# Kernel optimization log

Measured on AMD Instinct MI355X. Metric: run time of the kernel, lower is better.

## Reference

```python
import jax, jax.numpy as jnp
import numpy as np

B, S, E = 4, 2048, 1024
H = 16
DH = E // H  # per-head qk and v projection dim (64)


def setup_inputs() -> dict:
    key = jax.random.key(0)
    ks = jax.random.split(key, 12)
    sc = lambda fan_in: 1.0 / np.sqrt(fan_in)
    inp = {
        "query": jax.random.normal(ks[0], (B, S, E), jnp.float32),
        "key": jax.random.normal(ks[1], (B, S, E), jnp.float32),
        "value": jax.random.normal(ks[2], (B, S, E), jnp.float32),
        "attention_bias": jax.random.normal(ks[3], (S, S), jnp.float32),
        # stacked per-head Linear weights/biases (H independent heads in original)
        "Wq": jax.random.uniform(ks[4], (H, E, DH), jnp.float32, -sc(E), sc(E)),
        "bq": jax.random.uniform(ks[5], (H, DH), jnp.float32, -sc(E), sc(E)),
        "Wk": jax.random.uniform(ks[6], (H, E, DH), jnp.float32, -sc(E), sc(E)),
        "bk": jax.random.uniform(ks[7], (H, DH), jnp.float32, -sc(E), sc(E)),
        "Wv": jax.random.uniform(ks[8], (H, E, DH), jnp.float32, -sc(E), sc(E)),
        "bv": jax.random.uniform(ks[9], (H, DH), jnp.float32, -sc(E), sc(E)),
        "Wo": jax.random.uniform(ks[10], (H * DH, E), jnp.float32, -sc(H * DH), sc(H * DH)),
        "bo": jax.random.uniform(ks[11], (E,), jnp.float32, -sc(H * DH), sc(H * DH)),
    }
    return inp


def reference(query, key, value, attention_bias, Wq, bq, Wk, bk, Wv, bv, Wo, bo):
    # Batched equivalent of per-head Linear projections + per-head SDPA.
    q = jnp.einsum("bse,hed->bhsd", query, Wq) + bq[None, :, None, :]   # (B,H,S,DH)
    k = jnp.einsum("bte,hed->bhtd", key, Wk) + bk[None, :, None, :]     # (B,H,S,DH)
    v = jnp.einsum("bte,hed->bhtd", value, Wv) + bv[None, :, None, :]   # (B,H,S,DH)
    scale = 1.0 / jnp.sqrt(jnp.asarray(DH, q.dtype))
    scores = jnp.einsum("bhsd,bhtd->bhst", q, k) * scale                # (B,H,S,S)
    scores = scores + attention_bias[None, None, :, :]
    attn = jax.nn.softmax(scores, axis=-1)
    # dropout_p = 0.0 -> no dropout
    ctx = jnp.einsum("bhst,bhtd->bhsd", attn, v)                        # (B,H,S,DH)
    concat = ctx.transpose(0, 2, 1, 3).reshape(B, S, H * DH)            # (B,S,H*DH)
    return concat @ Wo + bo                                             # (B,S,E)
```

## Files before the change

### kernel.cpp

```cpp
#include <hip/hip_runtime.h>

#define S_LEN 2048
#define E_DIM 1024
#define H_NUM 16

typedef __attribute__((ext_vector_type(8))) short s16x8;
typedef __attribute__((ext_vector_type(4))) float f32x4;
typedef __attribute__((ext_vector_type(4))) _Float16 h16x4;

#define GA(p) ((__attribute__((address_space(1))) void*)(p))
#define LA(p) ((__attribute__((address_space(3))) void*)(p))

#define LOG2E 1.4426950408889634f
#define SCALE_Q (0.125f * LOG2E)
#define SHIFT 12.0f

union cvt16 { int4 v; s16x8 s8; short e[8]; };

__device__ __forceinline__ short f2bf(float f) {
  union { float f; unsigned u; } v; v.f = f;
  unsigned r = v.u + 0x7FFFu + ((v.u >> 16) & 1u);
  return (short)(r >> 16);
}
__device__ __forceinline__ short f2bf_fast(float f) {
  union { float f; unsigned u; } v; v.f = f;
  return (short)((v.u + 0x8000u) >> 16);
}

__global__ void transpose_cast(const float* __restrict__ src, short* __restrict__ dst,
                               int R, int C, long sbs, long dbs, float scale) {
  __shared__ float tile[32][33];
  const float* s = src + (long)blockIdx.z * sbs;
  short* d = dst + (long)blockIdx.z * dbs;
  int c0 = blockIdx.x * 32, r0 = blockIdx.y * 32;
  #pragma unroll
  for (int i = threadIdx.y; i < 32; i += 8)
    tile[i][threadIdx.x] = s[(long)(r0 + i) * C + c0 + threadIdx.x];
  __syncthreads();
  #pragma unroll
  for (int i = threadIdx.y; i < 32; i += 8)
    d[(long)(c0 + i) * R + r0 + threadIdx.x] = f2bf(tile[threadIdx.x][i] * scale);
}

__global__ void bias_rearrange(const float* __restrict__ bias, _Float16* __restrict__ biasR) {
  long tg = (long)blockIdx.x * 256 + threadIdx.x;
  long o = tg * 4;
  int q = (int)(o >> 11);
  int t = (int)(o & 2047);
  int b64 = t & ~63, u = t & 63, ln = u >> 2;
  const float* src = bias + (long)q * 2048 + b64 + ln;
  h16x4 hv;
  #pragma unroll
  for (int nt = 0; nt < 4; ++nt) hv[nt] = (_Float16)src[nt * 16];
  *(h16x4*)(biasR + o) = hv;
}

__global__ __launch_bounds__(256, 3) void proj_gemm(
    const float* __restrict__ Aq, const float* __restrict__ Ak, const float* __restrict__ Av,
    const short* __restrict__ Bt,
    const float* __restrict__ bq, const float* __restrict__ bk, const float* __restrict__ bv,
    short* __restrict__ qkOut, short* __restrict__ VT) {
  __shared__ float Asub[128 * 64];
  __shared__ short Bsub[128 * 64];
  const int tid = threadIdx.x;
  const int w = tid >> 6, lane = tid & 63, ln = lane & 15, quad = lane >> 4;
  const int row0 = blockIdx.x * 128, n0 = blockIdx.y * 128;
  const int seg = n0 >> 10;
  const float* A = (seg == 0) ? Aq : ((seg == 1) ? Ak : Av);
  const float* bptr = (seg == 0) ? bq : ((seg == 1) ? bk : bv);
  const float bscale = (seg == 0) ? SCALE_Q : 1.0f;
  const int nloc = n0 & 1023;
  const int wm = (w & 1) * 64, wn = (w >> 1) * 64;

  f32x4 acc[4][4];
  #pragma unroll
  for (int i = 0; i < 4; ++i)
    #pragma unroll
    for (int j = 0; j < 4; ++j) acc[i][j] = (f32x4){0.f, 0.f, 0.f, 0.f};

  for (int kt = 0; kt < 16; ++kt) {
    const int k0 = kt * 64;
    #pragma unroll
    for (int j = 0; j < 4; ++j) {
      int ci = (w * 4 + j) * 64 + lane;
      int r = ci >> 3, s = ci & 7, g = s ^ (r & 7);
      const short* gb = Bt + (long)(n0 + r) * 1024 + k0 + g * 8;
      __builtin_amdgcn_global_load_lds(GA(gb), LA(&Bsub[ci * 8]), 16, 0, 0);
    }
    #pragma unroll
    for (int it = 0; it < 8; ++it) {
      int ci = it * 256 + tid;
      int r = ci >> 4, s = ci & 15, g = (s & 8) | ((s & 7) ^ (r & 7));
      const float* ga = A + (long)(row0 + r) * 1024 + k0 + g * 4;
      __builtin_amdgcn_global_load_lds(GA(ga), LA(&Asub[ci * 4]), 16, 0, 0);
    }
    __syncthreads();
    #pragma unroll
    for (int kk = 0; kk < 2; ++kk) {
      s16x8 af[4], bfr[4];
      #pragma unroll
      for (int i = 0; i < 4; ++i) {
        int ra = wm + i * 16 + ln;
        int c0 = kk * 8 + quad * 2;
        int s0 = (c0 & 8) | ((c0 & 7) ^ (ra & 7));
        int c1 = c0 + 1;
        int s1 = (c1 & 8) | ((c1 & 7) ^ (ra & 7));
        f32x4 lo = *(const f32x4*)&Asub[ra * 64 + s0 * 4];
        f32x4 hi = *(const f32x4*)&Asub[ra * 64 + s1 * 4];
        s16x8 t;
        t[0] = f2bf(lo[0]); t[1] = f2bf(lo[1]); t[2] = f2bf(lo[2]); t[3] = f2bf(lo[3]);
        t[4] = f2bf(hi[0]); t[5] = f2bf(hi[1]); t[6] = f2bf(hi[2]); t[7] = f2bf(hi[3]);
        af[i] = t;
      }
      #pragma unroll
      for (int j = 0; j < 4; ++j) {
        int rb = wn + j * 16 + ln;
        int slot = (kk * 4 + quad) ^ (rb & 7);
        bfr[j] = *(const s16x8*)&Bsub[rb * 64 + slot * 8];
      }
      #pragma unroll
      for (int i = 0; i < 4; ++i)
        #pragma unroll
        for (int j = 0; j < 4; ++j)
          acc[i][j] = __builtin_amdgcn_mfma_f32_16x16x32_bf16(af[i], bfr[j], acc[i][j], 0, 0, 0);
    }
    __syncthreads();
  }
  if (seg < 2) {
    #pragma unroll
    for (int j = 0; j < 4; ++j) {
      float bvj = bptr[nloc + wn + j * 16 + ln] * bscale;
      int n = n0 + wn + j * 16 + ln;
      #pragma unroll
      for (int i = 0; i < 4; ++i)
        #pragma unroll
        for (int r = 0; r < 4; ++r) {
          int row = row0 + wm + i * 16 + quad * 4 + r;
          qkOut[(long)row * 2048 + n] = f2bf(acc[i][j][r] + bvj);
        }
    }
  } else {
    #pragma unroll
    for (int j = 0; j < 4; ++j) {
      int nl = nloc + wn + j * 16 + ln;
      int hh = nl >> 6, d = nl & 63;
      float bvj = bptr[nl];
      #pragma unroll
      for (int i = 0; i < 4; ++i) {
        int row = row0 + wm + i * 16 + quad * 4;
        int b = row >> 11, t = row & 2047;
        short4 sv;
        sv.x = f2bf(acc[i][j][0] + bvj);
        sv.y = f2bf(acc[i][j][1] + bvj);
        sv.z = f2bf(acc[i][j][2] + bvj);
        sv.w = f2bf(acc[i][j][3] + bvj);
        *(short4*)&VT[((long)(b * 16 + hh) * 64 + d) * 2048 + t] = sv;
      }
    }
  }
}

__global__ __launch_bounds__(256, 3) void flash_attn(
    const short* __restrict__ qk, const short* __restrict__ VT,
    const _Float16* __restrict__ biasR, short* __restrict__ concat) {
  __shared__ short Ks[2][4096];
  __shared__ short Vs[2][4096];
  __shared__ short Ps[128 * 72];
  const int tid = threadIdx.x;
  const int w = tid >> 6, lane = tid & 63, ln = lane & 15, quad = lane >> 4;
  const int q0 = blockIdx.x * 128;
  const int h = blockIdx.y, bb = blockIdx.z;

  s16x8 ones;
  #pragma unroll
  for (int e = 0; e < 8; ++e) ones[e] = (short)0x3F80;

  s16x8 qf[2][2];
  const short* qbase = qk + (long)(bb * 2048 + q0 + w * 32) * 2048 + h * 64;
  #pragma unroll
  for (int i = 0; i < 2; ++i)
    #pragma unroll
    for (int kk = 0; kk < 2; ++kk) {
      cvt16 u; u.v = *(const int4*)(qbase + (long)(i * 16 + ln) * 2048 + kk * 32 + quad * 8);
      qf[i][kk] = u.s8;
    }

  f32x4 o[2][4], lacc[2];
  #pragma unroll
  for (int i = 0; i < 2; ++i) {
    #pragma unroll
    for (int nt = 0; nt < 4; ++nt) o[i][nt] = (f32x4){0.f, 0.f, 0.f, 0.f};
    lacc[i] = (f32x4){0.f, 0.f, 0.f, 0.f};
  }

  const short* kbase = qk + (long)bb * 2048 * 2048 + 1024 + h * 64;
  const short* vbase = VT + (long)(bb * 16 + h) * 64 * 2048;
  const _Float16* bbase = biasR + (long)(q0 + w * 32 + quad * 4) * 2048 + ln * 4;

  #pragma unroll
  for (int j = 0; j < 2; ++j) {
    int ci = (w * 2 + j) * 64 + lane;
    int r = ci >> 3, cs = (ci & 7) ^ (r & 7);
    __builtin_amdgcn_global_load_lds(GA(kbase + (long)r * 2048 + cs * 8), LA(&Ks[0][(w * 2 + j) * 512]), 16, 0, 0);
    __builtin_amdgcn_global_load_lds(GA(vbase + (long)r * 2048 + cs * 8), LA(&Vs[0][(w * 2 + j) * 512]), 16, 0, 0);
  }

  for (int kv = 0; kv < 32; ++kv) {
    const int t0 = kv * 64, b = kv & 1;
    __syncthreads();

    h16x4 bld[2][4];
    #pragma unroll
    for (int i = 0; i < 2; ++i)
      #pragma unroll
      for (int r = 0; r < 4; ++r)
        bld[i][r] = *(const h16x4*)(bbase + (long)(i * 16 + r) * 2048 + t0);
    __builtin_amdgcn_sched_barrier(0);

    if (kv < 31) {
      const short* kb = kbase + (long)(t0 + 64) * 2048;
      const short* vb = vbase + (t0 + 64);
      #pragma unroll
      for (int j = 0; j < 2; ++j) {
        int ci = (w * 2 + j) * 64 + lane;
        int r = ci >> 3, cs = (ci & 7) ^ (r & 7);
        __builtin_amdgcn_global_load_lds(GA(kb + (long)r * 2048 + cs * 8), LA(&Ks[b ^ 1][(w * 2 + j) * 512]), 16, 0, 0);
        __builtin_amdgcn_global_load_lds(GA(vb + (long)r * 2048 + cs * 8), LA(&Vs[b ^ 1][(w * 2 + j) * 512]), 16, 0, 0);
      }
    }

    f32x4 sa[2][4];
    #pragma unroll
    for (int i = 0; i < 2; ++i)
      #pragma unroll
      for (int nt = 0; nt < 4; ++nt) sa[i][nt] = (f32x4){-SHIFT, -SHIFT, -SHIFT, -SHIFT};
    #pragma unroll
    for (int kk = 0; kk < 2; ++kk) {
      s16x8 bfr[4];
      #pragma unroll
      for (int nt = 0; nt < 4; ++nt)
        bfr[nt] = *(const s16x8*)&Ks[b][((nt * 16 + ln) << 6) + (((kk * 4 + quad) ^ (ln & 7)) << 3)];
      #pragma unroll
      for (int i = 0; i < 2; ++i)
        #pragma unroll
        for (int nt = 0; nt < 4; ++nt)
          sa[i][nt] = __builtin_amdgcn_mfma_f32_16x16x32_bf16(qf[i][kk], bfr[nt], sa[i][nt], 0, 0, 0);
    }

    #pragma unroll
    for (int i = 0; i < 2; ++i)
      #pragma unroll
      for (int r = 0; r < 4; ++r) {
        #pragma unroll
        for (int nt = 0; nt < 4; ++nt) {
          float bb_ = (float)bld[i][r][nt];
          float p = __builtin_amdgcn_exp2f(fmaf(bb_, LOG2E, sa[i][nt][r]));
          Ps[(w * 32 + i * 16 + quad * 4 + r) * 72 + nt * 16 + ln] = f2bf_fast(p);
        }
      }

    #pragma unroll
    for (int kk = 0; kk < 2; ++kk) {
      s16x8 pa[2], vbf[4];
      #pragma unroll
      for (int i = 0; i < 2; ++i)
        pa[i] = *(const s16x8*)&Ps[(w * 32 + i * 16 + ln) * 72 + kk * 32 + quad * 8];
      #pragma unroll
      for (int nt = 0; nt < 4; ++nt)
        vbf[nt] = *(const s16x8*)&Vs[b][((nt * 16 + ln) << 6) + (((kk * 4 + quad) ^ (ln & 7)) << 3)];
      #pragma unroll
      for (int i = 0; i < 2; ++i) {
        #pragma unroll
        for (int nt = 0; nt < 4; ++nt)
          o[i][nt] = __builtin_amdgcn_mfma_f32_16x16x32_bf16(pa[i], vbf[nt], o[i][nt], 0, 0, 0);
        lacc[i] = __builtin_amdgcn_mfma_f32_16x16x32_bf16(pa[i], ones, lacc[i], 0, 0, 0);
      }
    }
  }

  #pragma unroll
  for (int i = 0; i < 2; ++i) {
    float inv[4];
    #pragma unroll
    for (int r = 0; r < 4; ++r) inv[r] = __builtin_amdgcn_rcpf(lacc[i][r]);
    long rowb = (long)bb * 2048 + q0 + w * 32 + i * 16 + quad * 4;
    #pragma unroll
    for (int nt = 0; nt < 4; ++nt)
      #pragma unroll
      for (int r = 0; r < 4; ++r)
        concat[(rowb + r) * 1024 + h * 64 + nt * 16 + ln] = f2bf(o[i][nt][r] * inv[r]);
  }
}

__global__ __launch_bounds__(256, 3) void out_gemm(
    const short* __restrict__ A, const short* __restrict__ Bt,
    const float* __restrict__ bo, float* __restrict__ Cout) {
  __shared__ short Asub[128 * 64];
  __shared__ short Bsub[128 * 64];
  const int tid = threadIdx.x;
  const int w = tid >> 6, lane = tid & 63, ln = lane & 15, quad = lane >> 4;
  const int row0 = blockIdx.x * 128, n0 = blockIdx.y * 128;
  const int wm = (w & 1) * 64, wn = (w >> 1) * 64;

  f32x4 acc[4][4];
  #pragma unroll
  for (int i = 0; i < 4; ++i)
    #pragma unroll
    for (int j = 0; j < 4; ++j) acc[i][j] = (f32x4){0.f, 0.f, 0.f, 0.f};

  for (int kt = 0; kt < 16; ++kt) {
    const int k0 = kt * 64;
    #pragma unroll
    for (int j = 0; j < 4; ++j) {
      int ci = (w * 4 + j) * 64 + lane;
      int r = ci >> 3, s = ci & 7, g = s ^ (r & 7);
      const short* ga = A + (long)(row0 + r) * 1024 + k0 + g * 8;
      __builtin_amdgcn_global_load_lds(GA(ga), LA(&Asub[ci * 8]), 16, 0, 0);
      const short* gb = Bt + (long)(n0 + r) * 1024 + k0 + g * 8;
      __builtin_amdgcn_global_load_lds(GA(gb), LA(&Bsub[ci * 8]), 16, 0, 0);
    }
    __syncthreads();
    #pragma unroll
    for (int kk = 0; kk < 2; ++kk) {
      s16x8 af[4], bfr[4];
      #pragma unroll
      for (int i = 0; i < 4; ++i) {
        int ra = wm + i * 16 + ln;
        int slot = (kk * 4 + quad) ^ (ra & 7);
        af[i] = *(const s16x8*)&Asub[ra * 64 + slot * 8];
      }
      #pragma unroll
      for (int j = 0; j < 4; ++j) {
        int rb = wn + j * 16 + ln;
        int slot = (kk * 4 + quad) ^ (rb & 7);
        bfr[j] = *(const s16x8*)&Bsub[rb * 64 + slot * 8];
      }
      #pragma unroll
      for (int i = 0; i < 4; ++i)
        #pragma unroll
        for (int j = 0; j < 4; ++j)
          acc[i][j] = __builtin_amdgcn_mfma_f32_16x16x32_bf16(af[i], bfr[j], acc[i][j], 0, 0, 0);
    }
    __syncthreads();
  }
  #pragma unroll
  for (int j = 0; j < 4; ++j) {
    int n = n0 + wn + j * 16 + ln;
    float bvj = bo[n];
    #pragma unroll
    for (int i = 0; i < 4; ++i)
      #pragma unroll
      for (int r = 0; r < 4; ++r) {
        int row = row0 + wm + i * 16 + quad * 4 + r;
        Cout[(long)row * 1024 + n] = acc[i][j][r] + bvj;
      }
  }
}

extern "C" void kernel_launch(void* const* d_in, const int* in_sizes, int n_in,
                              void* d_out, int out_size, void* d_ws, size_t ws_size,
                              hipStream_t stream) {
  const float* query = (const float*)d_in[0];
  const float* key_  = (const float*)d_in[1];
  const float* value = (const float*)d_in[2];
  const float* abias = (const float*)d_in[3];
  const float* Wq = (const float*)d_in[4];
  const float* bq = (const float*)d_in[5];
  const float* Wk = (const float*)d_in[6];
  const float* bk = (const float*)d_in[7];
  const float* Wv = (const float*)d_in[8];
  const float* bv = (const float*)d_in[9];
  const float* Wo = (const float*)d_in[10];
  const float* bo = (const float*)d_in[11];
  float* out = (float*)d_out;

  char* ws = (char*)d_ws;
  short*    WqkvT  = (short*)(ws);
  _Float16* biasR  = (_Float16*)(ws);
  short*    qk     = (short*)(ws + 8388608);
  short*    VT     = (short*)(ws + 41943040);
  short*    WoT    = (short*)(ws + 41943040);
  short*    concat = (short*)(ws + 58720256);

  dim3 tb(32, 8);
  transpose_cast<<<dim3(2, 32, 16), tb, 0, stream>>>(Wq, WqkvT,           1024, 64, 65536L, 65536L, SCALE_Q);
  transpose_cast<<<dim3(2, 32, 16), tb, 0, stream>>>(Wk, WqkvT + 1048576, 1024, 64, 65536L, 65536L, 1.0f);
  transpose_cast<<<dim3(2, 32, 16), tb, 0, stream>>>(Wv, WqkvT + 2097152, 1024, 64, 65536L, 65536L, 1.0f);
  proj_gemm<<<dim3(64, 24), 256, 0, stream>>>(query, key_, value, WqkvT, bq, bk, bv, qk, VT);
  bias_rearrange<<<dim3(4096), 256, 0, stream>>>(abias, biasR);
  flash_attn<<<dim3(16, 16, 4), 256, 0, stream>>>(qk, VT, biasR, concat);
  transpose_cast<<<dim3(32, 32, 1), tb, 0, stream>>>(Wo, WoT, 1024, 1024, 0L, 0L, 1.0f);
  out_gemm<<<dim3(64, 8), 256, 0, stream>>>(concat, WoT, bo, out);
}
```

Baseline: 393.1 us.

## Keep softmax probabilities in registers by computing S^T and permuting V layout

Swaps MFMA operand order so the QK^T scores come out transposed, letting each lane pack its exponentiated probabilities directly into the bf16 A-operand for the PV MFMA instead of round-tripping through a shared-memory P buffer. To make this work, V's key positions are permuted within each 64-block in the projection epilogue, and the bias rearrangement is redone to match the new lane-to-element mapping, with wider vector loads. The removed LDS buffer allows raising the occupancy hint to 4 blocks, and s_setprio is added around MFMA bursts. Register pressure rises, and the intricate index permutations must stay consistent across kernels.

After: 442.0 us. +12.4%, slower.

```diff
diff --git a/kernel.cpp b/kernel.cpp
--- a/kernel.cpp
+++ b/kernel.cpp
@@ -7,6 +7,7 @@
 typedef __attribute__((ext_vector_type(8))) short s16x8;
 typedef __attribute__((ext_vector_type(4))) float f32x4;
 typedef __attribute__((ext_vector_type(4))) _Float16 h16x4;
+typedef __attribute__((ext_vector_type(8))) _Float16 h16x8;
 
 #define GA(p) ((__attribute__((address_space(1))) void*)(p))
 #define LA(p) ((__attribute__((address_space(3))) void*)(p))
@@ -25,6 +26,10 @@
 __device__ __forceinline__ short f2bf_fast(float f) {
   union { float f; unsigned u; } v; v.f = f;
   return (short)((v.u + 0x8000u) >> 16);
+}
+__device__ __forceinline__ unsigned pk2(float lo, float hi) {
+  return (unsigned)(unsigned short)f2bf_fast(lo) |
+         ((unsigned)(unsigned short)f2bf_fast(hi) << 16);
 }
 
 __global__ void transpose_cast(const float* __restrict__ src, short* __restrict__ dst,
@@ -43,16 +48,18 @@
 }
 
 __global__ void bias_rearrange(const float* __restrict__ bias, _Float16* __restrict__ biasR) {
-  long tg = (long)blockIdx.x * 256 + threadIdx.x;
-  long o = tg * 4;
-  int q = (int)(o >> 11);
-  int t = (int)(o & 2047);
-  int b64 = t & ~63, u = t & 63, ln = u >> 2;
-  const float* src = bias + (long)q * 2048 + b64 + ln;
-  h16x4 hv;
-  #pragma unroll
-  for (int nt = 0; nt < 4; ++nt) hv[nt] = (_Float16)src[nt * 16];
-  *(h16x4*)(biasR + o) = hv;
+  long g = (long)blockIdx.x * 256 + threadIdx.x;
+  int q    = (int)(g >> 8);
+  int kv   = ((int)(g >> 3)) & 31;
+  int quad = ((int)(g >> 1)) & 3;
+  int c    = (int)g & 1;
+  const float* src = bias + (long)q * 2048 + kv * 64 + c * 32 + quad * 4;
+  f32x4 lo = *(const f32x4*)(src);
+  f32x4 hi = *(const f32x4*)(src + 16);
+  h16x8 hv;
+  #pragma unroll
+  for (int e = 0; e < 4; ++e) { hv[e] = (_Float16)lo[e]; hv[4 + e] = (_Float16)hi[e]; }
+  *(h16x8*)(biasR + g * 8) = hv;
 }
 
 __global__ __launch_bounds__(256, 3) void proj_gemm(
@@ -149,23 +156,24 @@
       for (int i = 0; i < 4; ++i) {
         int row = row0 + wm + i * 16 + quad * 4;
         int b = row >> 11, t = row & 2047;
+        int u = t & 63;
+        int pt = (t & ~63) | (u & 0x23) | ((u & 0x10) >> 2) | ((u & 0x0C) << 1);
         short4 sv;
         sv.x = f2bf(acc[i][j][0] + bvj);
         sv.y = f2bf(acc[i][j][1] + bvj);
         sv.z = f2bf(acc[i][j][2] + bvj);
         sv.w = f2bf(acc[i][j][3] + bvj);
-        *(short4*)&VT[((long)(b * 16 + hh) * 64 + d) * 2048 + t] = sv;
-      }
-    }
-  }
-}
-
-__global__ __launch_bounds__(256, 3) void flash_attn(
+        *(short4*)&VT[((long)(b * 16 + hh) * 64 + d) * 2048 + pt] = sv;
+      }
+    }
+  }
+}
+
+__global__ __launch_bounds__(256, 4) void flash_attn(
     const short* __restrict__ qk, const short* __restrict__ VT,
     const _Float16* __restrict__ biasR, short* __restrict__ concat) {
   __shared__ short Ks[2][4096];
   __shared__ short Vs[2][4096];
-  __shared__ short Ps[128 * 72];
   const int tid = threadIdx.x;
   const int w = tid >> 6, lane = tid & 63, ln = lane & 15, quad = lane >> 4;
   const int q0 = blockIdx.x * 128;
@@ -195,7 +203,7 @@
 
   const short* kbase = qk + (long)bb * 2048 * 2048 + 1024 + h * 64;
   const short* vbase = VT + (long)(bb * 16 + h) * 64 * 2048;
-  const _Float16* bbase = biasR + (long)(q0 + w * 32 + quad * 4) * 2048 + ln * 4;
+  const _Float16* bbase = biasR + (long)(q0 + w * 32 + ln) * 2048 + quad * 16;
 
   #pragma unroll
   for (int j = 0; j < 2; ++j) {
@@ -209,12 +217,12 @@
     const int t0 = kv * 64, b = kv & 1;
     __syncthreads();
 
-    h16x4 bld[2][4];
+    h16x8 bld[2][2];
     #pragma unroll
     for (int i = 0; i < 2; ++i)
       #pragma unroll
-      for (int r = 0; r < 4; ++r)
-        bld[i][r] = *(const h16x4*)(bbase + (long)(i * 16 + r) * 2048 + t0);
+      for (int c = 0; c < 2; ++c)
+        bld[i][c] = *(const h16x8*)(bbase + (long)i * 16 * 2048 + kv * 64 + c * 8);
     __builtin_amdgcn_sched_barrier(0);
 
     if (kv < 31) {
@@ -240,41 +248,52 @@
       #pragma unroll
       for (int nt = 0; nt < 4; ++nt)
         bfr[nt] = *(const s16x8*)&Ks[b][((nt * 16 + ln) << 6) + (((kk * 4 + quad) ^ (ln & 7)) << 3)];
+      __builtin_amdgcn_s_setprio(1);
       #pragma unroll
       for (int i = 0; i < 2; ++i)
         #pragma unroll
         for (int nt = 0; nt < 4; ++nt)
-          sa[i][nt] = __builtin_amdgcn_mfma_f32_16x16x32_bf16(qf[i][kk], bfr[nt], sa[i][nt], 0, 0, 0);
-    }
-
-    #pragma unroll
-    for (int i = 0; i < 2; ++i)
-      #pragma unroll
-      for (int r = 0; r < 4; ++r) {
-        #pragma unroll
-        for (int nt = 0; nt < 4; ++nt) {
-          float bb_ = (float)bld[i][r][nt];
-          float p = __builtin_amdgcn_exp2f(fmaf(bb_, LOG2E, sa[i][nt][r]));
-          Ps[(w * 32 + i * 16 + quad * 4 + r) * 72 + nt * 16 + ln] = f2bf_fast(p);
+          sa[i][nt] = __builtin_amdgcn_mfma_f32_16x16x32_bf16(bfr[nt], qf[i][kk], sa[i][nt], 0, 0, 0);
+      __builtin_amdgcn_s_setprio(0);
+    }
+
+    s16x8 pa[2][2];
+    #pragma unroll
+    for (int i = 0; i < 2; ++i) {
+      #pragma unroll
+      for (int nt = 0; nt < 4; ++nt) {
+        #pragma unroll
+        for (int r = 0; r < 4; ++r) {
+          float bv = (float)bld[i][nt >> 1][(nt & 1) * 4 + r];
+          sa[i][nt][r] = __builtin_amdgcn_exp2f(fmaf(bv, LOG2E, sa[i][nt][r]));
         }
       }
+      #pragma unroll
+      for (int kk = 0; kk < 2; ++kk) {
+        union { unsigned u[4]; s16x8 v; } pw;
+        pw.u[0] = pk2(sa[i][2 * kk][0], sa[i][2 * kk][1]);
+        pw.u[1] = pk2(sa[i][2 * kk][2], sa[i][2 * kk][3]);
+        pw.u[2] = pk2(sa[i][2 * kk + 1][0], sa[i][2 * kk + 1][1]);
+        pw.u[3] = pk2(sa[i][2 * kk + 1][2], sa[i][2 * kk + 1][3]);
+        pa[i][kk] = pw.v;
+      }
+    }
 
     #pragma unroll
     for (int kk = 0; kk < 2; ++kk) {
-      s16x8 pa[2], vbf[4];
-      #pragma unroll
-      for (int i = 0; i < 2; ++i)
-        pa[i] = *(const s16x8*)&Ps[(w * 32 + i * 16 + ln) * 72 + kk * 32 + quad * 8];
+      s16x8 vbf[4];
       #pragma unroll
       for (int nt = 0; nt < 4; ++nt)
         vbf[nt] = *(const s16x8*)&Vs[b][((nt * 16 + ln) << 6) + (((kk * 4 + quad) ^ (ln & 7)) << 3)];
+      __builtin_amdgcn_s_setprio(1);
       #pragma unroll
       for (int i = 0; i < 2; ++i) {
         #pragma unroll
         for (int nt = 0; nt < 4; ++nt)
-          o[i][nt] = __builtin_amdgcn_mfma_f32_16x16x32_bf16(pa[i], vbf[nt], o[i][nt], 0, 0, 0);
-        lacc[i] = __builtin_amdgcn_mfma_f32_16x16x32_bf16(pa[i], ones, lacc[i], 0, 0, 0);
-      }
+          o[i][nt] = __builtin_amdgcn_mfma_f32_16x16x32_bf16(pa[i][kk], vbf[nt], o[i][nt], 0, 0, 0);
+        lacc[i] = __builtin_amdgcn_mfma_f32_16x16x32_bf16(pa[i][kk], ones, lacc[i], 0, 0, 0);
+      }
+      __builtin_amdgcn_s_setprio(0);
     }
   }
 
@@ -387,7 +406,7 @@
   transpose_cast<<<dim3(2, 32, 16), tb, 0, stream>>>(Wk, WqkvT + 1048576, 1024, 64, 65536L, 65536L, 1.0f);
   transpose_cast<<<dim3(2, 32, 16), tb, 0, stream>>>(Wv, WqkvT + 2097152, 1024, 64, 65536L, 65536L, 1.0f);
   proj_gemm<<<dim3(64, 24), 256, 0, stream>>>(query, key_, value, WqkvT, bq, bk, bv, qk, VT);
-  bias_rearrange<<<dim3(4096), 256, 0, stream>>>(abias, biasR);
+  bias_rearrange<<<dim3(2048), 256, 0, stream>>>(abias, biasR);
   flash_attn<<<dim3(16, 16, 4), 256, 0, stream>>>(qk, VT, biasR, concat);
   transpose_cast<<<dim3(32, 32, 1), tb, 0, stream>>>(Wo, WoT, 1024, 1024, 0L, 0L, 1.0f);
   out_gemm<<<dim3(64, 8), 256, 0, stream>>>(concat, WoT, bo, out);
```
